# Optimization experiments

Hardware: AMD Instinct MI355X
Metric: run time of the kernel (lower is better)

Reference implementation:

```python
import jax, jax.numpy as jnp
import numpy as np

N_NODES = 100000


def _gcn_layer(x, edge_index, W, b):
    # x: [N, Fin], edge_index: [2, E]
    row, col = edge_index[0], edge_index[1]
    n = x.shape[0]
    ones = jnp.ones(row.shape[0], dtype=x.dtype)
    deg = jax.ops.segment_sum(ones, row, num_segments=n)  # bincount(row)
    deg_inv_sqrt = jnp.where(deg > 0, deg ** -0.5, 0.0).astype(x.dtype)
    norm = deg_inv_sqrt[row] * deg_inv_sqrt[col]  # [E]
    h = x @ W + b  # linear first, as in the torch code
    # sparse COO matmul == scatter-add of norm-scaled source features into row
    msgs = norm[:, None] * h[col]  # [E, Fout]
    return jax.ops.segment_sum(msgs, row, num_segments=n)


def setup_inputs() -> dict:
    key = jax.random.key(0)
    ks = jax.random.split(key, 7)
    N, Fin, H, Fout = N_NODES, 256, 64, 64
    Epos, Eneg = 1600000, 1600000
    x = jax.random.normal(ks[0], (N, Fin), dtype=jnp.float32)
    pos_edge_index = jax.random.randint(ks[1], (2, Epos), 0, N, dtype=jnp.int64)
    neg_edge_index = jax.random.randint(ks[2], (2, Eneg), 0, N, dtype=jnp.int64)
    W1 = jax.random.normal(ks[3], (Fin, H), dtype=jnp.float32) * (1.0 / np.sqrt(Fin))
    b1 = jax.random.normal(ks[4], (H,), dtype=jnp.float32) * 0.01
    W2 = jax.random.normal(ks[5], (H, Fout), dtype=jnp.float32) * (1.0 / np.sqrt(H))
    b2 = jax.random.normal(ks[6], (Fout,), dtype=jnp.float32) * 0.01
    return {"x": x, "pos_edge_index": pos_edge_index, "neg_edge_index": neg_edge_index,
            "W1": W1, "b1": b1, "W2": W2, "b2": b2}


def reference(x, pos_edge_index, neg_edge_index, W1, b1, W2, b2):
    # encode: two GCN layers over pos_edge_index.
    # Note: the original calls self.PairNorm(x) but discards the result,
    # so PairNorm has no effect on the output.
    h = jax.nn.relu(_gcn_layer(x, pos_edge_index, W1, b1))
    z = _gcn_layer(h, pos_edge_index, W2, b2)  # [N, 64]
    # decode: dot product over concatenated pos+neg edges
    edge = jnp.concatenate([pos_edge_index, neg_edge_index], axis=-1)  # [2, Ep+En]
    return jnp.sum(z[edge[0]] * z[edge[1]], axis=-1)  # [Ep+En]
```

## Files before the change

kernel.cpp:

```cpp
#include <hip/hip_runtime.h>
#include <hip/hip_fp16.h>

#define FIN 256
#define FH  64
#define SCAN_BLK 1024
#define NCHUNK 8


__global__ __launch_bounds__(256) void deg_kernel(const int* __restrict__ rows,
                                                  unsigned* __restrict__ deg, int E) {
    int e = blockIdx.x * 256 + threadIdx.x;
    if (e < E) atomicAdd(&deg[rows[e]], 1u);
}


__global__ __launch_bounds__(256) void scan_block_kernel(const unsigned* __restrict__ deg,
                                                         int* __restrict__ rowptr,
                                                         int* __restrict__ blocksums, int N) {
    __shared__ int wsum[4];
    const int t = threadIdx.x;
    const int base = blockIdx.x * SCAN_BLK + t * 4;
    int d0 = 0, d1 = 0, d2 = 0, d3 = 0;
    if (base + 0 < N) d0 = (int)deg[base + 0];
    if (base + 1 < N) d1 = (int)deg[base + 1];
    if (base + 2 < N) d2 = (int)deg[base + 2];
    if (base + 3 < N) d3 = (int)deg[base + 3];
    const int tot = d0 + d1 + d2 + d3;
    const int lane = t & 63, wv = t >> 6;
    int inc = tot;
#pragma unroll
    for (int off = 1; off < 64; off <<= 1) {
        int v = __shfl_up(inc, off, 64);
        if (lane >= off) inc += v;
    }
    if (lane == 63) wsum[wv] = inc;
    __syncthreads();
    int woff = 0;
    for (int w = 0; w < wv; ++w) woff += wsum[w];
    const int ex = woff + inc - tot;
    if (base + 0 < N) rowptr[base + 0] = ex;
    if (base + 1 < N) rowptr[base + 1] = ex + d0;
    if (base + 2 < N) rowptr[base + 2] = ex + d0 + d1;
    if (base + 3 < N) rowptr[base + 3] = ex + d0 + d1 + d2;
    if (t == 255) blocksums[blockIdx.x] = woff + inc;
}


__global__ __launch_bounds__(256) void scan_add_kernel(int* __restrict__ rowptr,
                                                       int* __restrict__ cursor,
                                                       const unsigned* __restrict__ deg,
                                                       float* __restrict__ dis,
                                                       const int* __restrict__ blocksums,
                                                       int nb, int N, int E) {
    __shared__ int pre;
    const int t = threadIdx.x;
    const int i0 = blockIdx.x * 256;
    const int c0 = i0 / SCAN_BLK;
    if (t == 0) {
        int s = 0;
        for (int k = 0; k < c0; ++k) s += blocksums[k];
        pre = s;
    }
    __syncthreads();
    int i = i0 + t;
    if (i < N) {
        int v = rowptr[i] + pre;
        rowptr[i] = v;
        cursor[i] = v;
        unsigned d = deg[i];
        dis[i] = d ? 1.0f / sqrtf((float)d) : 0.0f;
    }
    if (i == 0) rowptr[N] = E;
}


__global__ __launch_bounds__(256) void scatter_edges_kernel(const int* __restrict__ rows,
                                                            const int* __restrict__ cols,
                                                            int* __restrict__ cursor,
                                                            int* __restrict__ colOut,
                                                            int* __restrict__ einv,
                                                            float chunk_scale, int E) {
    const int chunk = blockIdx.x & (NCHUNK - 1);
    const int eb = blockIdx.x >> 3;
    int e = eb * 256 + threadIdx.x;
    if (e >= E) return;
    int r = rows[e];
    int rc = (int)((float)r * chunk_scale);
    rc = rc > (NCHUNK - 1) ? (NCHUNK - 1) : rc;
    if (rc == chunk) {
        int p = atomicAdd(&cursor[r], 1);
        colOut[p] = cols[e];
        einv[p] = e;
    }
}


__global__ __launch_bounds__(256) void gemm1_kernel(const float* __restrict__ x,
                                                    const float* __restrict__ W,
                                                    const float* __restrict__ b,
                                                    const float* __restrict__ dis,
                                                    __half2* __restrict__ outh, int N) {
    __shared__ float xs[32][132];
    __shared__ float ws[32][64];
    const int t = threadIdx.x;
    const int rb = blockIdx.x * 128;
    const int rg = t >> 3, cg = t & 7;
    const int r0 = rg * 4, c0 = cg * 8;
    float acc[4][8];
#pragma unroll
    for (int i = 0; i < 4; ++i)
#pragma unroll
        for (int j = 0; j < 8; ++j) acc[i][j] = 0.f;

    const float4* x4 = (const float4*)x;
    const int kk = (t & 7) * 4;
    const int rloc = t >> 3;

    for (int k0 = 0; k0 < FIN; k0 += 32) {
        __syncthreads();
        {
            const float4* w4 = (const float4*)(W + k0 * 64);
            float4* wl = (float4*)&ws[0][0];
            wl[t]       = w4[t];
            wl[t + 256] = w4[t + 256];
        }
#pragma unroll
        for (int p = 0; p < 4; ++p) {
            int r = rloc + p * 32;
            int gr = rb + r; if (gr >= N) gr = N - 1;
            float4 v = x4[gr * 64 + (k0 >> 2) + (t & 7)];
            xs[kk + 0][r] = v.x; xs[kk + 1][r] = v.y;
            xs[kk + 2][r] = v.z; xs[kk + 3][r] = v.w;
        }
        __syncthreads();
#pragma unroll
        for (int k = 0; k < 32; ++k) {
            float4 xa = *(const float4*)&xs[k][r0];
            float4 wa = *(const float4*)&ws[k][c0];
            float4 wb = *(const float4*)&ws[k][c0 + 4];
            float xr[4] = {xa.x, xa.y, xa.z, xa.w};
            float wr[8] = {wa.x, wa.y, wa.z, wa.w, wb.x, wb.y, wb.z, wb.w};
#pragma unroll
            for (int i = 0; i < 4; ++i)
#pragma unroll
                for (int j = 0; j < 8; ++j) acc[i][j] = fmaf(xr[i], wr[j], acc[i][j]);
        }
    }
    float bias[8];
#pragma unroll
    for (int j = 0; j < 8; ++j) bias[j] = b[c0 + j];
#pragma unroll
    for (int i = 0; i < 4; ++i) {
        int gr = rb + r0 + i;
        if (gr < N) {
            float d = dis[gr];
            __half2 o[4];
            o[0] = __floats2half2_rn((acc[i][0] + bias[0]) * d, (acc[i][1] + bias[1]) * d);
            o[1] = __floats2half2_rn((acc[i][2] + bias[2]) * d, (acc[i][3] + bias[3]) * d);
            o[2] = __floats2half2_rn((acc[i][4] + bias[4]) * d, (acc[i][5] + bias[5]) * d);
            o[3] = __floats2half2_rn((acc[i][6] + bias[6]) * d, (acc[i][7] + bias[7]) * d);
            *(uint4*)&outh[gr * 32 + (c0 >> 1)] = *(uint4*)o;
        }
    }
}


__global__ __launch_bounds__(256) void gather16_kernel(const int* __restrict__ rowptr,
                                                       const int* __restrict__ cols,
                                                       const float4* __restrict__ h4,
                                                       const float* __restrict__ dscale,
                                                       float* __restrict__ outf,
                                                       __half2* __restrict__ outh,
                                                       int N, int tohalf) {
    const int t = threadIdx.x;
    int r = blockIdx.x * 8 + (t >> 5);
    if (r >= N) return;
    const int l32 = t & 31;
    const int l8 = t & 7;
    const int g4 = (t >> 3) & 3;
    const int rowbase = t & 32;
    int s = rowptr[r], e = rowptr[r + 1];

    float2 acc[4];
#pragma unroll
    for (int k = 0; k < 4; ++k) { acc[k].x = 0.f; acc[k].y = 0.f; }

    for (int base = s; base < e; base += 32) {
        int n = e - base; if (n > 32) n = 32;
        int idx = (l32 < n) ? cols[base + l32] : 0;
        for (int j = 0; j < n; j += 8) {
            int pos0 = j + g4, pos1 = j + 4 + g4;
            bool a0 = pos0 < n, a1 = pos1 < n;
            int c0 = __shfl(idx, rowbase + (a0 ? pos0 : 0));
            int c1 = __shfl(idx, rowbase + (a1 ? pos1 : 0));
            float4 v0 = h4[(size_t)c0 * 8 + l8];
            float4 v1 = h4[(size_t)c1 * 8 + l8];
            union { float4 f; __half2 h[4]; } u0, u1;
            u0.f = v0; u1.f = v1;
            if (a0) {
#pragma unroll
                for (int k = 0; k < 4; ++k) {
                    float2 f = __half22float2(u0.h[k]);
                    acc[k].x += f.x; acc[k].y += f.y;
                }
            }
            if (a1) {
#pragma unroll
                for (int k = 0; k < 4; ++k) {
                    float2 f = __half22float2(u1.h[k]);
                    acc[k].x += f.x; acc[k].y += f.y;
                }
            }
        }
    }
#pragma unroll
    for (int k = 0; k < 4; ++k) {
        acc[k].x += __shfl_xor(acc[k].x, 8);
        acc[k].y += __shfl_xor(acc[k].y, 8);
        acc[k].x += __shfl_xor(acc[k].x, 16);
        acc[k].y += __shfl_xor(acc[k].y, 16);
    }
    if (g4 == 0) {
        if (tohalf) {
            float d = dscale[r];
            __half2 o[4];
#pragma unroll
            for (int k = 0; k < 4; ++k)
                o[k] = __floats2half2_rn(acc[k].x * d, acc[k].y * d);
            *(uint4*)&outh[(size_t)r * 32 + l8 * 4] = *(uint4*)o;
        } else {
            float4 o0, o1;
            o0.x = acc[0].x; o0.y = acc[0].y; o0.z = acc[1].x; o0.w = acc[1].y;
            o1.x = acc[2].x; o1.y = acc[2].y; o1.z = acc[3].x; o1.w = acc[3].y;
            *(float4*)&outf[(size_t)r * 64 + l8 * 8]     = o0;
            *(float4*)&outf[(size_t)r * 64 + l8 * 8 + 4] = o1;
        }
    }
}


__global__ __launch_bounds__(256) void gemm2_kernel(const float* __restrict__ agg,
                                                    const float* __restrict__ dis,
                                                    const float* __restrict__ W,
                                                    const float* __restrict__ b,
                                                    __half2* __restrict__ outh, int N) {
    __shared__ float xs[64][132];
    __shared__ float ws[64][64];
    const int t = threadIdx.x;
    const int rb = blockIdx.x * 128;
    {
        const float4* w4 = (const float4*)W;
        float4* wl = (float4*)&ws[0][0];
#pragma unroll
        for (int p = 0; p < 4; ++p) wl[p * 256 + t] = w4[p * 256 + t];
    }
    {
        const float4* a4 = (const float4*)agg;
        const int c4 = (t & 15) * 4;
        const int rloc = t >> 4;
#pragma unroll
        for (int p = 0; p < 8; ++p) {
            int r = rloc + p * 16;
            int gr = rb + r; if (gr >= N) gr = N - 1;
            float d = dis[gr];
            float4 v = a4[gr * 16 + (t & 15)];
            xs[c4 + 0][r] = fmaxf(v.x * d, 0.f);
            xs[c4 + 1][r] = fmaxf(v.y * d, 0.f);
            xs[c4 + 2][r] = fmaxf(v.z * d, 0.f);
            xs[c4 + 3][r] = fmaxf(v.w * d, 0.f);
        }
    }
    __syncthreads();
    const int rg = t >> 3, cg = t & 7;
    const int r0 = rg * 4, c0 = cg * 8;
    float acc[4][8];
#pragma unroll
    for (int i = 0; i < 4; ++i)
#pragma unroll
        for (int j = 0; j < 8; ++j) acc[i][j] = 0.f;
#pragma unroll 16
    for (int k = 0; k < 64; ++k) {
        float4 xa = *(const float4*)&xs[k][r0];
        float4 wa = *(const float4*)&ws[k][c0];
        float4 wb = *(const float4*)&ws[k][c0 + 4];
        float xr[4] = {xa.x, xa.y, xa.z, xa.w};
        float wr[8] = {wa.x, wa.y, wa.z, wa.w, wb.x, wb.y, wb.z, wb.w};
#pragma unroll
        for (int i = 0; i < 4; ++i)
#pragma unroll
            for (int j = 0; j < 8; ++j) acc[i][j] = fmaf(xr[i], wr[j], acc[i][j]);
    }
    float bias[8];
#pragma unroll
    for (int j = 0; j < 8; ++j) bias[j] = b[c0 + j];
#pragma unroll
    for (int i = 0; i < 4; ++i) {
        int gr = rb + r0 + i;
        if (gr < N) {
            float d = dis[gr];
            __half2 o[4];
            o[0] = __floats2half2_rn((acc[i][0] + bias[0]) * d, (acc[i][1] + bias[1]) * d);
            o[1] = __floats2half2_rn((acc[i][2] + bias[2]) * d, (acc[i][3] + bias[3]) * d);
            o[2] = __floats2half2_rn((acc[i][4] + bias[4]) * d, (acc[i][5] + bias[5]) * d);
            o[3] = __floats2half2_rn((acc[i][6] + bias[6]) * d, (acc[i][7] + bias[7]) * d);
            *(uint4*)&outh[gr * 32 + (c0 >> 1)] = *(uint4*)o;
        }
    }
}


__device__ __forceinline__ float dot8h(float4 A, float4 B) {
    union { float4 f; __half2 h[4]; } ua, ub;
    ua.f = A; ub.f = B;
    float s = 0.f;
#pragma unroll
    for (int k = 0; k < 4; ++k) {
        float2 fa = __half22float2(ua.h[k]);
        float2 fb = __half22float2(ub.h[k]);
        s = fmaf(fa.x, fb.x, s);
        s = fmaf(fa.y, fb.y, s);
    }
    return s;
}

__global__ __launch_bounds__(256) void decode16_kernel(const int* __restrict__ rowptr,
                                                       const int* __restrict__ cols,
                                                       const int* __restrict__ einv,
                                                       const int* __restrict__ ne,
                                                       const float4* __restrict__ zf4,
                                                       float* __restrict__ outp,
                                                       int N, int negB, int Ep, int En) {
    const int t = threadIdx.x;
    const int l8 = t & 7;

    if ((int)blockIdx.x < negB) {
        const int g = t >> 3;
        const int base = blockIdx.x * 256;
        int a[8], b[8];
        bool v[8];
#pragma unroll
        for (int q = 0; q < 8; ++q) {
            int e = base + q * 32 + g;
            v[q] = e < En;
            a[q] = 0; b[q] = 0;
            if (v[q]) { a[q] = ne[e]; b[q] = ne[En + e]; }
        }
        float4 va[8], vb[8];
#pragma unroll
        for (int q = 0; q < 8; ++q) {
            va[q] = zf4[(size_t)a[q] * 8 + l8];
            vb[q] = zf4[(size_t)b[q] * 8 + l8];
        }
#pragma unroll
        for (int q = 0; q < 8; ++q) {
            float p = dot8h(va[q], vb[q]);
            p += __shfl_xor(p, 4);
            p += __shfl_xor(p, 2);
            p += __shfl_xor(p, 1);
            int e = base + q * 32 + g;
            if (v[q] && l8 == 0) outp[Ep + e] = p;
        }
    } else {
        int r = (blockIdx.x - negB) * 8 + (t >> 5);
        if (r >= N) return;
        const int l32 = t & 31;
        const int rowbase = t & 32;
        const int g4 = (t >> 3) & 3;
        int s = rowptr[r], e = rowptr[r + 1];
        if (s == e) return;
        float zr8[8];
        {
            union { float4 f; __half2 h[4]; } uz;
            uz.f = zf4[(size_t)r * 8 + l8];
#pragma unroll
            for (int k = 0; k < 4; ++k) {
                float2 f = __half22float2(uz.h[k]);
                zr8[2 * k] = f.x; zr8[2 * k + 1] = f.y;
            }
        }
        for (int base = s; base < e; base += 32) {
            int n = e - base; if (n > 32) n = 32;
            int idx = (l32 < n) ? cols[base + l32] : 0;
            int ei  = (l32 < n) ? einv[base + l32] : 0;
            for (int j = 0; j < n; j += 8) {
                int pos0 = j + g4, pos1 = j + 4 + g4;
                bool a0 = pos0 < n, a1 = pos1 < n;
                int c0 = __shfl(idx, rowbase + (a0 ? pos0 : 0));
                int c1 = __shfl(idx, rowbase + (a1 ? pos1 : 0));
                int d0 = __shfl(ei, rowbase + (a0 ? pos0 : 0));
                int d1 = __shfl(ei, rowbase + (a1 ? pos1 : 0));
                float4 v0 = zf4[(size_t)c0 * 8 + l8];
                float4 v1 = zf4[(size_t)c1 * 8 + l8];
                union { float4 f; __half2 h[4]; } u0, u1;
                u0.f = v0; u1.f = v1;
                float p0 = 0.f, p1 = 0.f;
#pragma unroll
                for (int k = 0; k < 4; ++k) {
                    float2 f0 = __half22float2(u0.h[k]);
                    float2 f1 = __half22float2(u1.h[k]);
                    p0 = fmaf(zr8[2 * k], f0.x, p0); p0 = fmaf(zr8[2 * k + 1], f0.y, p0);
                    p1 = fmaf(zr8[2 * k], f1.x, p1); p1 = fmaf(zr8[2 * k + 1], f1.y, p1);
                }
                p0 += __shfl_xor(p0, 4); p0 += __shfl_xor(p0, 2); p0 += __shfl_xor(p0, 1);
                p1 += __shfl_xor(p1, 4); p1 += __shfl_xor(p1, 2); p1 += __shfl_xor(p1, 1);
                if (l8 == 0) {
                    if (a0) outp[d0] = p0;
                    if (a1) outp[d1] = p1;
                }
            }
        }
    }
}


extern "C" void kernel_launch(void* const* d_in, const int* in_sizes, int n_in,
                              void* d_out, int out_size, void* d_ws, size_t ws_size,
                              hipStream_t stream) {
    const float* x  = (const float*)d_in[0];
    const int*   pe = (const int*)d_in[1];
    const int*   ne = (const int*)d_in[2];
    const float* W1 = (const float*)d_in[3];
    const float* b1 = (const float*)d_in[4];
    const float* W2 = (const float*)d_in[5];
    const float* b2 = (const float*)d_in[6];
    float* outp = (float*)d_out;

    const int N  = in_sizes[0] / FIN;
    const int Ep = in_sizes[1] / 2;
    const int En = in_sizes[2] / 2;

    char* w = (char*)d_ws;
    size_t off = 0;
    auto alloc = [&](size_t bytes) {
        void* p = w + off;
        off = (off + bytes + 255) & ~(size_t)255;
        return p;
    };
    unsigned* deg   = (unsigned*)alloc((size_t)N * 4);
    float* dis      = (float*)alloc((size_t)N * 4);
    int* rowptr     = (int*)alloc((size_t)(N + 1) * 4);
    int* cursor     = (int*)alloc((size_t)N * 4);
    int* blocksums  = (int*)alloc(((size_t)N / SCAN_BLK + 2) * 4);
    int* colsorted  = (int*)alloc((size_t)Ep * 4);
    int* einv       = (int*)alloc((size_t)Ep * 4);
    __half2* A16    = (__half2*)alloc((size_t)N * 64 * 2);
    float* B        = (float*)alloc((size_t)N * 64 * 4);

    const int nscan = (N + SCAN_BLK - 1) / SCAN_BLK;
    const int nEdgeBlocks = (Ep + 255) / 256;

    hipMemsetAsync(deg, 0, (size_t)N * 4, stream);

    deg_kernel<<<nEdgeBlocks, 256, 0, stream>>>(pe, deg, Ep);
    scan_block_kernel<<<nscan, 256, 0, stream>>>(deg, rowptr, blocksums, N);
    scan_add_kernel<<<(N + 255) / 256, 256, 0, stream>>>(rowptr, cursor, deg, dis,
                                                         blocksums, nscan, N, Ep);
    scatter_edges_kernel<<<nEdgeBlocks * NCHUNK, 256, 0, stream>>>(
        pe, pe + Ep, cursor, colsorted, einv, (float)NCHUNK / (float)N, Ep);
    gemm1_kernel<<<(N + 127) / 128, 256, 0, stream>>>(x, W1, b1, dis, A16, N);
    gather16_kernel<<<(N + 7) / 8, 256, 0, stream>>>(rowptr, colsorted, (const float4*)A16,
                                                     nullptr, B, nullptr, N, 0);
    gemm2_kernel<<<(N + 127) / 128, 256, 0, stream>>>(B, dis, W2, b2, A16, N);
    __half2* z16 = (__half2*)B;
    gather16_kernel<<<(N + 7) / 8, 256, 0, stream>>>(rowptr, colsorted, (const float4*)A16,
                                                     dis, nullptr, z16, N, 1);
    const int negB = (En + 255) / 256;
    const int posB = (N + 7) / 8;
    decode16_kernel<<<negB + posB, 256, 0, stream>>>(rowptr, colsorted, einv, ne,
                                                     (const float4*)z16, outp,
                                                     N, negB, Ep, En);
}
```

Before: 510.0 us.

## Fuse edge scatter and first GEMM into one interleaved launch

Merges the CSR edge-scatter kernel and the first dense GEMM into a single launch. Blocks are grouped in 512s: the first 8 of each group do GEMM tiles and the rest do scatter work. The atomic-heavy, latency-bound scatter can then overlap with the compute-bound GEMM on the same GPU, and one launch is removed. Scatter blocks now reserve the GEMM's shared memory, which may reduce their occupancy.

```diff
diff --git a/kernel.cpp b/kernel.cpp
--- a/kernel.cpp
+++ b/kernel.cpp
@@ -74,36 +74,40 @@
 }
 
 
-__global__ __launch_bounds__(256) void scatter_edges_kernel(const int* __restrict__ rows,
-                                                            const int* __restrict__ cols,
-                                                            int* __restrict__ cursor,
-                                                            int* __restrict__ colOut,
-                                                            int* __restrict__ einv,
-                                                            float chunk_scale, int E) {
-    const int chunk = blockIdx.x & (NCHUNK - 1);
-    const int eb = blockIdx.x >> 3;
-    int e = eb * 256 + threadIdx.x;
-    if (e >= E) return;
-    int r = rows[e];
-    int rc = (int)((float)r * chunk_scale);
-    rc = rc > (NCHUNK - 1) ? (NCHUNK - 1) : rc;
-    if (rc == chunk) {
-        int p = atomicAdd(&cursor[r], 1);
-        colOut[p] = cols[e];
-        einv[p] = e;
-    }
-}
-
-
-__global__ __launch_bounds__(256) void gemm1_kernel(const float* __restrict__ x,
-                                                    const float* __restrict__ W,
-                                                    const float* __restrict__ b,
-                                                    const float* __restrict__ dis,
-                                                    __half2* __restrict__ outh, int N) {
+__global__ __launch_bounds__(256) void scatter_gemm1_kernel(
+        const int* __restrict__ rows, const int* __restrict__ cols,
+        int* __restrict__ cursor, int* __restrict__ colOut, int* __restrict__ einv,
+        float chunk_scale, int E,
+        const float* __restrict__ x, const float* __restrict__ W1,
+        const float* __restrict__ b1, const float* __restrict__ dis,
+        __half2* __restrict__ outh, int N, int gemmB, int scatterB) {
     __shared__ float xs[32][132];
     __shared__ float ws[32][64];
     const int t = threadIdx.x;
-    const int rb = blockIdx.x * 128;
+    const int grp = blockIdx.x >> 9;
+    const int wofs = blockIdx.x & 511;
+
+    if (wofs >= 8) {
+        const int sIdx = blockIdx.x - 8 * (grp + 1);
+        if (sIdx >= scatterB) return;
+        const int chunk = sIdx & (NCHUNK - 1);
+        const int eb = sIdx >> 3;
+        int e = eb * 256 + t;
+        if (e >= E) return;
+        int r = rows[e];
+        int rc = (int)((float)r * chunk_scale);
+        rc = rc > (NCHUNK - 1) ? (NCHUNK - 1) : rc;
+        if (rc == chunk) {
+            int p = atomicAdd(&cursor[r], 1);
+            colOut[p] = cols[e];
+            einv[p] = e;
+        }
+        return;
+    }
+
+    const int gb = grp * 8 + wofs;
+    if (gb >= gemmB) return;
+    const int rb = gb * 128;
     const int rg = t >> 3, cg = t & 7;
     const int r0 = rg * 4, c0 = cg * 8;
     float acc[4][8];
@@ -119,7 +123,7 @@
     for (int k0 = 0; k0 < FIN; k0 += 32) {
         __syncthreads();
         {
-            const float4* w4 = (const float4*)(W + k0 * 64);
+            const float4* w4 = (const float4*)(W1 + k0 * 64);
             float4* wl = (float4*)&ws[0][0];
             wl[t]       = w4[t];
             wl[t + 256] = w4[t + 256];
@@ -148,7 +152,7 @@
     }
     float bias[8];
 #pragma unroll
-    for (int j = 0; j < 8; ++j) bias[j] = b[c0 + j];
+    for (int j = 0; j < 8; ++j) bias[j] = b1[c0 + j];
 #pragma unroll
     for (int i = 0; i < 4; ++i) {
         int gr = rb + r0 + i;
@@ -455,9 +459,15 @@
     scan_block_kernel<<<nscan, 256, 0, stream>>>(deg, rowptr, blocksums, N);
     scan_add_kernel<<<(N + 255) / 256, 256, 0, stream>>>(rowptr, cursor, deg, dis,
                                                          blocksums, nscan, N, Ep);
-    scatter_edges_kernel<<<nEdgeBlocks * NCHUNK, 256, 0, stream>>>(
-        pe, pe + Ep, cursor, colsorted, einv, (float)NCHUNK / (float)N, Ep);
-    gemm1_kernel<<<(N + 127) / 128, 256, 0, stream>>>(x, W1, b1, dis, A16, N);
+    const int scatterB = nEdgeBlocks * NCHUNK;
+    const int gemmB = (N + 127) / 128;
+    int ngroups = (scatterB + 503) / 504;
+    const int ng2 = (gemmB + 7) / 8;
+    if (ngroups < ng2) ngroups = ng2;
+    const int T = scatterB + 8 * ngroups;
+    scatter_gemm1_kernel<<<T, 256, 0, stream>>>(pe, pe + Ep, cursor, colsorted, einv,
+                                                (float)NCHUNK / (float)N, Ep,
+                                                x, W1, b1, dis, A16, N, gemmB, scatterB);
     gather16_kernel<<<(N + 7) / 8, 256, 0, stream>>>(rowptr, colsorted, (const float4*)A16,
                                                      nullptr, B, nullptr, N, 0);
     gemm2_kernel<<<(N + 127) / 128, 256, 0, stream>>>(B, dis, W2, b2, A16, N);
```

Result: slower. 577.6 us (+13.3%).
